# Optimization experiments

Hardware: AMD Instinct MI355X
Metric: run time of the kernel (lower is better)

## Reference

```python
import jax, jax.numpy as jnp
import numpy as np

D_K = 64

def setup_inputs() -> dict:
    key = jax.random.key(0)
    kx, kq, kk, kv = jax.random.split(key, 4)
    B, T, D = 4, 2048, 1024
    s = 1.0 / np.sqrt(D)
    return {
        "x": jax.random.normal(kx, (B, T, D), dtype=jnp.float32),
        "Wq": jax.random.normal(kq, (D, D_K), dtype=jnp.float32) * s,
        "Wk": jax.random.normal(kk, (D, D_K), dtype=jnp.float32) * s,
        "Wv": jax.random.normal(kv, (D, D_K), dtype=jnp.float32) * s,
    }

def reference(x, Wq, Wk, Wv):
    # x: [B, T, D]; Wq/Wk/Wv: [D, d_k]
    Q = x @ Wq  # [B, T, d_k]
    K = x @ Wk
    V = x @ Wv
    scale = 1.0 / jnp.sqrt(jnp.asarray(Q.shape[-1], Q.dtype))
    scores = jnp.einsum('btd,bsd->bts', Q, K) * scale  # [B, T, T]
    T = scores.shape[-1]
    causal = jnp.tril(jnp.ones((T, T), dtype=bool))  # keep lower-tri incl diag
    masked = jnp.where(causal, scores, -jnp.inf)
    attn = jax.nn.softmax(masked, axis=-1)  # dropout p=0.0 -> identity
    context = jnp.einsum('bts,bsd->btd', attn, V)  # [B, T, d_k]
    return context
```

## Files before the change

### kernel.cpp

```cpp
#include <hip/hip_runtime.h>
#include <math.h>

#define BT    8192
#define TSEQ  2048
#define DIN   1024
#define DK    64

typedef __attribute__((ext_vector_type(8))) short bf16x8;
typedef __attribute__((ext_vector_type(4))) short bf16x4;
typedef __attribute__((ext_vector_type(4))) float f32x4;

static __device__ inline unsigned short f2bf(float f) {
    union { float f; unsigned u; } v; v.f = f;
    unsigned r = v.u + 0x7fff + ((v.u >> 16) & 1);
    return (unsigned short)(r >> 16);
}

static __device__ inline bf16x4 cvt4(float4 a) {
    bf16x4 r;
    r[0] = (short)f2bf(a.x); r[1] = (short)f2bf(a.y);
    r[2] = (short)f2bf(a.z); r[3] = (short)f2bf(a.w);
    return r;
}

__global__ __launch_bounds__(256) void wt_kernel(
    const float* __restrict__ Wq, const float* __restrict__ Wk,
    const float* __restrict__ Wv, unsigned short* __restrict__ WT)
{
    __shared__ float ws[64][65];
    const int tid = threadIdx.x;
    const int mat = blockIdx.x >> 4;
    const int k0  = (blockIdx.x & 15) << 6;
    const float* W = (mat == 0) ? Wq : ((mat == 1) ? Wk : Wv);

    const int j = tid & 63;
    for (int i = tid >> 6; i < 64; i += 4)
        ws[i][j] = W[(size_t)(k0 + i) * DK + j];
    __syncthreads();

    const int n  = tid & 63;
    const int c0 = (tid >> 6) << 4;
    unsigned short* dst = WT + (size_t)(mat * 64 + n) * DIN + k0 + c0;
    #pragma unroll
    for (int c = 0; c < 16; ++c) dst[c] = f2bf(ws[c0 + c][n]);
}

__global__ __launch_bounds__(256, 2) void proj_kernel(
    const float* __restrict__ x, const unsigned short* __restrict__ WT,
    unsigned short* __restrict__ Qb, unsigned short* __restrict__ Kb,
    unsigned short* __restrict__ VT)
{
    __shared__ unsigned short xs[16][1032];
    __shared__ unsigned short wtb[192][72];
    const int tid = threadIdx.x;
    const int m0 = blockIdx.x * 16;

    {
        const int r = tid >> 4;
        const int c = (tid & 15) << 2;
        const float* src = x + (size_t)(m0 + r) * DIN + c;
        float4 tmp[16];
        #pragma unroll
        for (int s = 0; s < 16; ++s) tmp[s] = *(const float4*)(src + s * 64);
        #pragma unroll
        for (int s = 0; s < 16; ++s) *(bf16x4*)&xs[r][c + s * 64] = cvt4(tmp[s]);
    }

    const int lane = tid & 63;
    const int w    = tid >> 6;
    const int lr = lane & 15, lg = lane >> 4;

    f32x4 acc[3];
    #pragma unroll
    for (int nt = 0; nt < 3; ++nt) acc[nt] = (f32x4){0.f, 0.f, 0.f, 0.f};

    __syncthreads();

    for (int kc = 0; kc < 16; ++kc) {
        const int k0 = kc << 6;

        #pragma unroll
        for (int i = 0; i < 6; ++i) {
            const int c = tid + i * 256;
            const int n = c >> 3;
            const int sl = c & 7;
            *(bf16x8*)&wtb[n][((sl + n) & 7) << 3] =
                *(const bf16x8*)(WT + (size_t)n * DIN + k0 + (sl << 3));
        }
        __syncthreads();

        #pragma unroll
        for (int st = 0; st < 2; ++st) {
            const bf16x8 af = *(const bf16x8*)&xs[lr][k0 + (st << 5) + (lg << 3)];
            #pragma unroll
            for (int nt = 0; nt < 3; ++nt) {
                const int n = w * 48 + nt * 16 + lr;
                const int sl = (st << 2) + lg;
                const bf16x8 bf = *(const bf16x8*)&wtb[n][((sl + n) & 7) << 3];
                acc[nt] = __builtin_amdgcn_mfma_f32_16x16x32_bf16(af, bf, acc[nt], 0, 0, 0);
            }
        }
        __syncthreads();
    }

    const float qsc = 0.125f * 1.44269504088896340736f;
    #pragma unroll
    for (int nt = 0; nt < 3; ++nt) {
        const int gct = w * 3 + nt;
        #pragma unroll
        for (int r = 0; r < 4; ++r) {
            const int row = m0 + (lg << 2) + r;
            const float vv = acc[nt][r];
            if (gct < 4) {
                Qb[(size_t)row * DK + gct * 16 + lr] = f2bf(vv * qsc);
            } else if (gct < 8) {
                Kb[(size_t)row * DK + (gct - 4) * 16 + lr] = f2bf(vv);
            } else {
                const int d = (gct - 8) * 16 + lr;
                VT[((size_t)(row >> 11) * DK + d) * TSEQ + (row & (TSEQ - 1))] = f2bf(vv);
            }
        }
    }
}

__global__ __launch_bounds__(256, 2) void attn_kernel(
    const unsigned short* __restrict__ Qb, const unsigned short* __restrict__ Kb,
    const unsigned short* __restrict__ VT, float* __restrict__ O)
{
    __shared__ __align__(16) unsigned short P_lds[4][16][72];
    __shared__ float Opart[4][16][68];
    __shared__ float mpart[4][16];
    __shared__ float Lpart[4][16];

    const int lane = threadIdx.x & 63;
    const int w    = threadIdx.x >> 6;
    const int qt = ((blockIdx.x & 3) << 7) | (127 - (blockIdx.x >> 2));
    const int q0 = qt << 4;
    const int t0 = q0 & (TSEQ - 1);
    const int b  = q0 >> 11;
    const int lr = lane & 15;
    const int lg = lane >> 4;

    const unsigned short* Qrow = Qb + (size_t)(q0 + lr) * DK + (lg << 3);
    const bf16x8 qf0 = *(const bf16x8*)(Qrow);
    const bf16x8 qf1 = *(const bf16x8*)(Qrow + 32);

    const unsigned short* Kbase = Kb + (size_t)b * TSEQ * DK;
    const unsigned short* Vbase = VT + (size_t)b * DK * TSEQ;

    f32x4 oacc[4];
    #pragma unroll
    for (int dt = 0; dt < 4; ++dt) oacc[dt] = (f32x4){0.f, 0.f, 0.f, 0.f};
    float m[4] = {-INFINITY, -INFINITY, -INFINITY, -INFINITY};
    float L[4] = {0.f, 0.f, 0.f, 0.f};

    const int nkb = (t0 >> 6) + 1;
    for (int kb = w; kb < nkb; kb += 4) {
        const int s0 = kb << 6;

        f32x4 s[4];
        #pragma unroll
        for (int ct = 0; ct < 4; ++ct) {
            const unsigned short* Krow =
                Kbase + (size_t)(s0 + ct * 16 + lr) * DK + (lg << 3);
            const bf16x8 k0 = *(const bf16x8*)(Krow);
            const bf16x8 k1 = *(const bf16x8*)(Krow + 32);
            f32x4 a = (f32x4){0.f, 0.f, 0.f, 0.f};
            a = __builtin_amdgcn_mfma_f32_16x16x32_bf16(qf0, k0, a, 0, 0, 0);
            a = __builtin_amdgcn_mfma_f32_16x16x32_bf16(qf1, k1, a, 0, 0, 0);
            s[ct] = a;
        }

        bf16x8 vf0[4], vf1[4];
        #pragma unroll
        for (int dt = 0; dt < 4; ++dt) {
            const unsigned short* Vrow =
                Vbase + (size_t)(dt * 16 + lr) * TSEQ + s0 + (lg << 3);
            vf0[dt] = *(const bf16x8*)(Vrow);
            vf1[dt] = *(const bf16x8*)(Vrow + 32);
        }

        if (kb == nkb - 1) {
            #pragma unroll
            for (int ct = 0; ct < 4; ++ct)
                #pragma unroll
                for (int r = 0; r < 4; ++r)
                    if (s0 + ct * 16 + lr > t0 + lg * 4 + r) s[ct][r] = -INFINITY;
        }

        float tmax[4];
        #pragma unroll
        for (int r = 0; r < 4; ++r)
            tmax[r] = fmaxf(fmaxf(s[0][r], s[1][r]), fmaxf(s[2][r], s[3][r]));
        #pragma unroll
        for (int off = 1; off < 16; off <<= 1)
            #pragma unroll
            for (int r = 0; r < 4; ++r)
                tmax[r] = fmaxf(tmax[r], __shfl_xor(tmax[r], off));

        float f[4];
        #pragma unroll
        for (int r = 0; r < 4; ++r) {
            const float mn = fmaxf(m[r], tmax[r]);
            f[r] = exp2f(m[r] - mn);
            m[r] = mn;
        }

        float ps[4] = {0.f, 0.f, 0.f, 0.f};
        unsigned short pb[4][4];
        #pragma unroll
        for (int ct = 0; ct < 4; ++ct)
            #pragma unroll
            for (int r = 0; r < 4; ++r) {
                const float p = exp2f(s[ct][r] - m[r]);
                ps[r] += p;
                pb[ct][r] = f2bf(p);
            }
        #pragma unroll
        for (int r = 0; r < 4; ++r) L[r] = L[r] * f[r] + ps[r];
        #pragma unroll
        for (int r = 0; r < 4; ++r) {
            oacc[0][r] *= f[r]; oacc[1][r] *= f[r];
            oacc[2][r] *= f[r]; oacc[3][r] *= f[r];
        }

        #pragma unroll
        for (int ct = 0; ct < 4; ++ct)
            #pragma unroll
            for (int r = 0; r < 4; ++r)
                P_lds[w][lg * 4 + r][ct * 16 + lr] = pb[ct][r];
        asm volatile("s_waitcnt lgkmcnt(0)" ::: "memory");
        const bf16x8 pf0 = *(const bf16x8*)&P_lds[w][lr][(lg << 3)];
        const bf16x8 pf1 = *(const bf16x8*)&P_lds[w][lr][32 + (lg << 3)];

        #pragma unroll
        for (int dt = 0; dt < 4; ++dt) {
            oacc[dt] = __builtin_amdgcn_mfma_f32_16x16x32_bf16(pf0, vf0[dt], oacc[dt], 0, 0, 0);
            oacc[dt] = __builtin_amdgcn_mfma_f32_16x16x32_bf16(pf1, vf1[dt], oacc[dt], 0, 0, 0);
        }
    }

    #pragma unroll
    for (int off = 1; off < 16; off <<= 1)
        #pragma unroll
        for (int r = 0; r < 4; ++r) L[r] += __shfl_xor(L[r], off);

    #pragma unroll
    for (int dt = 0; dt < 4; ++dt)
        #pragma unroll
        for (int r = 0; r < 4; ++r)
            Opart[w][(lg << 2) + r][dt * 16 + lr] = oacc[dt][r];
    if (lr == 0) {
        #pragma unroll
        for (int r = 0; r < 4; ++r) {
            mpart[w][(lg << 2) + r] = m[r];
            Lpart[w][(lg << 2) + r] = L[r];
        }
    }
    __syncthreads();

    #pragma unroll
    for (int r = 0; r < 4; ++r) {
        const int row = (lg << 2) + r;
        const float M = fmaxf(fmaxf(mpart[0][row], mpart[1][row]),
                              fmaxf(mpart[2][row], mpart[3][row]));
        float Lf = 0.f, o = 0.f;
        #pragma unroll
        for (int v = 0; v < 4; ++v) {
            const float fv = exp2f(mpart[v][row] - M);
            Lf += fv * Lpart[v][row];
            o  += fv * Opart[v][row][(w << 4) + lr];
        }
        O[(size_t)(q0 + row) * DK + (w << 4) + lr] = o / Lf;
    }
}

extern "C" void kernel_launch(void* const* d_in, const int* in_sizes, int n_in,
                              void* d_out, int out_size, void* d_ws, size_t ws_size,
                              hipStream_t stream) {
    const float* x  = (const float*)d_in[0];
    const float* Wq = (const float*)d_in[1];
    const float* Wk = (const float*)d_in[2];
    const float* Wv = (const float*)d_in[3];
    float* O = (float*)d_out;

    unsigned short* Qb = (unsigned short*)d_ws;
    unsigned short* Kb = Qb + (size_t)BT * DK;
    unsigned short* VT = Kb + (size_t)BT * DK;
    unsigned short* WT = VT + (size_t)BT * DK;

    wt_kernel  <<<dim3(48),  dim3(256), 0, stream>>>(Wq, Wk, Wv, WT);
    proj_kernel<<<dim3(512), dim3(256), 0, stream>>>(x, WT, Qb, Kb, VT);
    attn_kernel<<<dim3(512), dim3(256), 0, stream>>>(Qb, Kb, VT, O);
}
```

Before: 51.78 us.

## Prefetch next K tile into registers and skip softmax rescale when max stays near

Loads the K fragments for the next key block one iteration ahead, so the QK^T MFMAs no longer wait on fresh global loads. Adds a lazy-rescale path: the row max reduction across lanes, the exp correction and the rescale of the O and L accumulators run only when some row's tile max exceeds the running max by more than a threshold. This cuts shuffles and per-iteration multiplies in the inner loop. It costs extra registers for the prefetched K fragments and lets probabilities grow up to 2^8 before rescaling, which is fine in fp32 but could reduce occupancy.

```diff
diff --git a/kernel.cpp b/kernel.cpp
--- a/kernel.cpp
+++ b/kernel.cpp
@@ -155,19 +155,28 @@
     float L[4] = {0.f, 0.f, 0.f, 0.f};
 
     const int nkb = (t0 >> 6) + 1;
-    for (int kb = w; kb < nkb; kb += 4) {
-        const int s0 = kb << 6;
-
-        f32x4 s[4];
+
+    bf16x8 kf0[4], kf1[4];
+    if (w < nkb) {
+        const int s0 = w << 6;
         #pragma unroll
         for (int ct = 0; ct < 4; ++ct) {
             const unsigned short* Krow =
                 Kbase + (size_t)(s0 + ct * 16 + lr) * DK + (lg << 3);
-            const bf16x8 k0 = *(const bf16x8*)(Krow);
-            const bf16x8 k1 = *(const bf16x8*)(Krow + 32);
+            kf0[ct] = *(const bf16x8*)(Krow);
+            kf1[ct] = *(const bf16x8*)(Krow + 32);
+        }
+    }
+
+    for (int kb = w; kb < nkb; kb += 4) {
+        const int s0 = kb << 6;
+
+        f32x4 s[4];
+        #pragma unroll
+        for (int ct = 0; ct < 4; ++ct) {
             f32x4 a = (f32x4){0.f, 0.f, 0.f, 0.f};
-            a = __builtin_amdgcn_mfma_f32_16x16x32_bf16(qf0, k0, a, 0, 0, 0);
-            a = __builtin_amdgcn_mfma_f32_16x16x32_bf16(qf1, k1, a, 0, 0, 0);
+            a = __builtin_amdgcn_mfma_f32_16x16x32_bf16(qf0, kf0[ct], a, 0, 0, 0);
+            a = __builtin_amdgcn_mfma_f32_16x16x32_bf16(qf1, kf1[ct], a, 0, 0, 0);
             s[ct] = a;
         }
 
@@ -180,6 +189,18 @@
             vf1[dt] = *(const bf16x8*)(Vrow + 32);
         }
 
+        bf16x8 nk0[4], nk1[4];
+        if (kb + 4 < nkb) {
+            const int sn = (kb + 4) << 6;
+            #pragma unroll
+            for (int ct = 0; ct < 4; ++ct) {
+                const unsigned short* Krow =
+                    Kbase + (size_t)(sn + ct * 16 + lr) * DK + (lg << 3);
+                nk0[ct] = *(const bf16x8*)(Krow);
+                nk1[ct] = *(const bf16x8*)(Krow + 32);
+            }
+        }
+
         if (kb == nkb - 1) {
             #pragma unroll
             for (int ct = 0; ct < 4; ++ct)
@@ -188,22 +209,40 @@
                     if (s0 + ct * 16 + lr > t0 + lg * 4 + r) s[ct][r] = -INFINITY;
         }
 
-        float tmax[4];
+        float pm[4];
         #pragma unroll
         for (int r = 0; r < 4; ++r)
-            tmax[r] = fmaxf(fmaxf(s[0][r], s[1][r]), fmaxf(s[2][r], s[3][r]));
-        #pragma unroll
-        for (int off = 1; off < 16; off <<= 1)
-            #pragma unroll
-            for (int r = 0; r < 4; ++r)
-                tmax[r] = fmaxf(tmax[r], __shfl_xor(tmax[r], off));
-
-        float f[4];
-        #pragma unroll
-        for (int r = 0; r < 4; ++r) {
-            const float mn = fmaxf(m[r], tmax[r]);
-            f[r] = exp2f(m[r] - mn);
-            m[r] = mn;
+            pm[r] = fmaxf(fmaxf(s[0][r], s[1][r]), fmaxf(s[2][r], s[3][r]));
+
+        bool near = true;
+        #pragma unroll
+        for (int r = 0; r < 4; ++r)
+            near = near && (pm[r] - m[r] <= 8.0f);
+
+        if (!__all(near)) {
+            float tmax[4];
+            #pragma unroll
+            for (int r = 0; r < 4; ++r) tmax[r] = pm[r];
+            #pragma unroll
+            for (int off = 1; off < 16; off <<= 1)
+                #pragma unroll
+                for (int r = 0; r < 4; ++r)
+                    tmax[r] = fmaxf(tmax[r], __shfl_xor(tmax[r], off));
+
+            float f[4];
+            #pragma unroll
+            for (int r = 0; r < 4; ++r) {
+                const float mn = fmaxf(m[r], tmax[r]);
+                f[r] = exp2f(m[r] - mn);
+                m[r] = mn;
+            }
+            #pragma unroll
+            for (int r = 0; r < 4; ++r) L[r] *= f[r];
+            #pragma unroll
+            for (int r = 0; r < 4; ++r) {
+                oacc[0][r] *= f[r]; oacc[1][r] *= f[r];
+                oacc[2][r] *= f[r]; oacc[3][r] *= f[r];
+            }
         }
 
         float ps[4] = {0.f, 0.f, 0.f, 0.f};
@@ -217,12 +256,7 @@
                 pb[ct][r] = f2bf(p);
             }
         #pragma unroll
-        for (int r = 0; r < 4; ++r) L[r] = L[r] * f[r] + ps[r];
-        #pragma unroll
-        for (int r = 0; r < 4; ++r) {
-            oacc[0][r] *= f[r]; oacc[1][r] *= f[r];
-            oacc[2][r] *= f[r]; oacc[3][r] *= f[r];
-        }
+        for (int r = 0; r < 4; ++r) L[r] += ps[r];
 
         #pragma unroll
         for (int ct = 0; ct < 4; ++ct)
@@ -238,6 +272,9 @@
             oacc[dt] = __builtin_amdgcn_mfma_f32_16x16x32_bf16(pf0, vf0[dt], oacc[dt], 0, 0, 0);
             oacc[dt] = __builtin_amdgcn_mfma_f32_16x16x32_bf16(pf1, vf1[dt], oacc[dt], 0, 0, 0);
         }
+
+        #pragma unroll
+        for (int ct = 0; ct < 4; ++ct) { kf0[ct] = nk0[ct]; kf1[ct] = nk1[ct]; }
     }
 
     #pragma unroll
```

Result: no change. 51.18 us (-1.2%).
